# Kernel optimization log

Measured on AMD Instinct MI355X. Metric: run time of the kernel, lower is better.

The kernel has to match this reference:

```python
import jax, jax.numpy as jnp
import numpy as np

N, E = 50000, 800000
DIN, DH, DOUT, HEADS = 128, 128, 128, 4
NEG_SLOPE = 0.2
LN_EPS = 1e-5


def setup_inputs() -> dict:
    key = jax.random.key(0)
    ks = jax.random.split(key, 20)
    s = 0.05
    inp = {
        "x": jax.random.normal(ks[0], (N, DIN), jnp.float32),
        "edge_index": jax.random.randint(ks[1], (2, E), 0, N, jnp.int32),
        "W_in": jax.random.normal(ks[2], (DIN, DH), jnp.float32) * s,
        "b_in": jnp.zeros((DH,), jnp.float32),
        # GAT layer 0 (heads=4, concat)
        "W0": jax.random.normal(ks[3], (DH, DH), jnp.float32) * s,
        "as0": jax.random.normal(ks[4], (HEADS, DH // HEADS), jnp.float32) * s,
        "ad0": jax.random.normal(ks[5], (HEADS, DH // HEADS), jnp.float32) * s,
        "b0": jnp.zeros((DH,), jnp.float32),
        # GAT layer 1 (heads=4, concat)
        "W1": jax.random.normal(ks[6], (DH, DH), jnp.float32) * s,
        "as1": jax.random.normal(ks[7], (HEADS, DH // HEADS), jnp.float32) * s,
        "ad1": jax.random.normal(ks[8], (HEADS, DH // HEADS), jnp.float32) * s,
        "b1": jnp.zeros((DH,), jnp.float32),
        # GAT layer 2 (heads=1, no concat)
        "W2": jax.random.normal(ks[9], (DH, DOUT), jnp.float32) * s,
        "as2": jax.random.normal(ks[10], (1, DOUT), jnp.float32) * s,
        "ad2": jax.random.normal(ks[11], (1, DOUT), jnp.float32) * s,
        "b2": jnp.zeros((DOUT,), jnp.float32),
    }
    return inp


def layer_norm(x):
    mu = jnp.mean(x, -1, keepdims=True)
    var = jnp.var(x, -1, keepdims=True)
    return (x - mu) * jax.lax.rsqrt(var + LN_EPS)


def gat_conv(x, src, dst, W, a_src, a_dst, bias, heads, concat):
    # x: [N, D_in]; src/dst include self-loops
    n = x.shape[0]
    c = W.shape[1] // heads
    h = (x @ W).reshape(n, heads, c)                       # [N,H,C]
    al_s = jnp.sum(h * a_src[None], -1)                    # [N,H]
    al_d = jnp.sum(h * a_dst[None], -1)                    # [N,H]
    e = jax.nn.leaky_relu(al_s[src] + al_d[dst], NEG_SLOPE)  # [Etot,H]
    m = jax.ops.segment_max(e, dst, num_segments=n)
    ex = jnp.exp(e - m[dst])
    z = jax.ops.segment_sum(ex, dst, num_segments=n)
    alpha = ex / (z[dst] + 1e-16)                          # [Etot,H]
    out = jax.ops.segment_sum(h[src] * alpha[:, :, None], dst, num_segments=n)  # [N,H,C]
    out = out.reshape(n, heads * c) if concat else jnp.mean(out, 1)
    return out + bias


def reference(x, edge_index, W_in, b_in, W0, as0, ad0, b0,
              W1, as1, ad1, b1, W2, as2, ad2, b2):
    n = x.shape[0]
    loop = jnp.arange(n, dtype=edge_index.dtype)
    src = jnp.concatenate([edge_index[0], loop])  # PyG GATConv adds self-loops
    dst = jnp.concatenate([edge_index[1], loop])

    h = jax.nn.relu(x @ W_in + b_in)  # dropout is identity in eval mode

    res = h
    h = gat_conv(h, src, dst, W0, as0, ad0, b0, HEADS, True)
    h = layer_norm(jax.nn.elu(h) + res)

    res = h
    h = gat_conv(h, src, dst, W1, as1, ad1, b1, HEADS, True)
    h = layer_norm(jax.nn.elu(h) + res)

    h = gat_conv(h, src, dst, W2, as2, ad2, b2, 1, False)
    return layer_norm(h)
```

## Files before the change

### kernel.cpp

```cpp
#include <hip/hip_runtime.h>
#include <hip/hip_bf16.h>

typedef unsigned short ushort_t;
typedef unsigned int uint_t;
typedef __attribute__((ext_vector_type(8))) short short8;
typedef __attribute__((ext_vector_type(4))) float f32x4;
typedef __attribute__((ext_vector_type(2))) float f32x2;

__device__ __forceinline__ ushort_t f2bf(float f) {
    uint_t u = __float_as_uint(f);
    uint_t r = (u + 0x7FFFu + ((u >> 16) & 1u)) >> 16;
    return (ushort_t)r;
}
__device__ __forceinline__ float bf2f_lo(uint_t u) { return __uint_as_float(u << 16); }
__device__ __forceinline__ float bf2f_hi(uint_t u) { return __uint_as_float(u & 0xffff0000u); }
__device__ __forceinline__ f32x2 bf2x2(uint_t u) {
    f32x2 r;
    r.x = __uint_as_float(u << 16);
    r.y = __uint_as_float(u);
    return r;
}
__device__ __forceinline__ f32x2 pk_fma(f32x2 a, f32x2 b, f32x2 c) {
    f32x2 d;
    asm("v_pk_fma_f32 %0, %1, %2, %3" : "=v"(d) : "v"(a), "v"(b), "v"(c));
    return d;
}

#define BSH 8
#define BCK 256
#define CSR_CAP 6144
#define EPB 4096

__global__ void prep_kernel(const float* __restrict__ W_in,
                            const float* __restrict__ W0, const float* __restrict__ as0,
                            const float* __restrict__ ad0,
                            const float* __restrict__ W1, const float* __restrict__ as1,
                            const float* __restrict__ ad1,
                            const float* __restrict__ W2, const float* __restrict__ as2,
                            const float* __restrict__ ad2,
                            ushort_t* __restrict__ BfIn, ushort_t* __restrict__ Bf0,
                            ushort_t* __restrict__ Bf1, ushort_t* __restrict__ Bf2,
                            const int* __restrict__ ei, int* __restrict__ bhist,
                            int E, int N) {
    __shared__ int hist[256];
    int b = blockIdx.x;
    if (b < 35) {
        const float *W, *a_s, *a_d;
        ushort_t* Bf;
        int H, NT, nt;
        if (b < 8)       { W = W_in; a_s = nullptr; a_d = nullptr; Bf = BfIn; H = 0; NT = 8; nt = b; }
        else if (b < 17) { W = W0; a_s = as0; a_d = ad0; Bf = Bf0; H = 4; NT = 9; nt = b - 8; }
        else if (b < 26) { W = W1; a_s = as1; a_d = ad1; Bf = Bf1; H = 4; NT = 9; nt = b - 17; }
        else             { W = W2; a_s = as2; a_d = ad2; Bf = Bf2; H = 1; NT = 9; nt = b - 26; }
        int l = threadIdx.x & 63;
        int ks = threadIdx.x >> 6;
        int kb = ks * 32 + (l >> 4) * 8;
        int col = l & 15;
        ushort_t v[8];
        if (nt < 8) {
#pragma unroll
            for (int j = 0; j < 8; ++j)
                v[j] = f2bf(W[(size_t)(kb + j) * 128 + nt * 16 + col]);
        } else {
#pragma unroll
            for (int j = 0; j < 8; ++j) {
                int k = kb + j;
                float s = 0.f;
                if (H == 4) {
                    if (col < 4) {
                        for (int c = 0; c < 32; ++c)
                            s += W[(size_t)k * 128 + col * 32 + c] * a_s[col * 32 + c];
                    } else if (col < 8) {
                        int h = col - 4;
                        for (int c = 0; c < 32; ++c)
                            s += W[(size_t)k * 128 + h * 32 + c] * a_d[h * 32 + c];
                    }
                } else {
                    if (col == 0) {
                        for (int c = 0; c < 128; ++c) s += W[(size_t)k * 128 + c] * a_s[c];
                    } else if (col == 1) {
                        for (int c = 0; c < 128; ++c) s += W[(size_t)k * 128 + c] * a_d[c];
                    }
                }
                v[j] = f2bf(s);
            }
        }
        uint4 u;
        u.x = (uint_t)v[0] | ((uint_t)v[1] << 16);
        u.y = (uint_t)v[2] | ((uint_t)v[3] << 16);
        u.z = (uint_t)v[4] | ((uint_t)v[5] << 16);
        u.w = (uint_t)v[6] | ((uint_t)v[7] << 16);
        *(uint4*)(Bf + ((size_t)(ks * NT + nt) * 64 + l) * 8) = u;
    } else {
        int tid = threadIdx.x;
        int blk = b - 35;
        hist[tid] = 0;
        __syncthreads();
        int base = blk * EPB;
        int Etot = E + N;
#pragma unroll
        for (int r = 0; r < EPB / 256; ++r) {
            int i = base + r * 256 + tid;
            if (i < Etot) {
                int dst = (i < E) ? ei[E + i] : (i - E);
                atomicAdd(&hist[dst >> BSH], 1);
            }
        }
        __syncthreads();
        bhist[blk * 256 + tid] = hist[tid];
    }
}

__global__ void csr_scan1(const int* __restrict__ bhist, int* __restrict__ obase,
                          int* __restrict__ gtot, int NBLK) {
    __shared__ int ws[4];
    int b = blockIdx.x;
    int t = threadIdx.x;
    int v = (t < NBLK) ? bhist[t * 256 + b] : 0;
    int lane = t & 63, w = t >> 6;
    int x = v;
#pragma unroll
    for (int off = 1; off < 64; off <<= 1) {
        int t2 = __shfl_up(x, off, 64);
        if (lane >= off) x += t2;
    }
    if (lane == 63) ws[w] = x;
    __syncthreads();
    int add = 0;
    for (int j = 0; j < w; ++j) add += ws[j];
    int excl = add + x - v;
    if (t < NBLK) obase[t * 256 + b] = excl;
    if (t == 255) gtot[b] = excl + v;
}

__global__ void csr_scan2(const int* __restrict__ gtot, int* __restrict__ gbase,
                          int* __restrict__ rowp, int N, int Etot) {
    __shared__ int ws[4];
    int t = threadIdx.x;
    int v = gtot[t];
    int lane = t & 63, w = t >> 6;
    int x = v;
#pragma unroll
    for (int off = 1; off < 64; off <<= 1) {
        int t2 = __shfl_up(x, off, 64);
        if (lane >= off) x += t2;
    }
    if (lane == 63) ws[w] = x;
    __syncthreads();
    int add = 0;
    for (int j = 0; j < w; ++j) add += ws[j];
    gbase[t] = add + x - v;
    if (t == 0) {
        gbase[256] = Etot;
        rowp[N] = Etot;
    }
}

__global__ void csr_scatter(const int* __restrict__ ei, const int* __restrict__ gbase,
                            const int* __restrict__ obase, uint2* __restrict__ pairs,
                            int E, int N) {
    __shared__ int cur[256];
    int tid = threadIdx.x;
    int blk = blockIdx.x;
    cur[tid] = gbase[tid] + obase[blk * 256 + tid];
    __syncthreads();
    int base = blk * EPB;
    int Etot = E + N;
#pragma unroll
    for (int r = 0; r < EPB / 256; ++r) {
        int i = base + r * 256 + tid;
        if (i < Etot) {
            int src = (i < E) ? ei[i] : (i - E);
            int dst = (i < E) ? ei[E + i] : (i - E);
            int pos = atomicAdd(&cur[dst >> BSH], 1);
            uint2 p;
            p.x = (uint_t)src;
            p.y = (uint_t)dst;
            pairs[pos] = p;
        }
    }
}

__global__ void bucket_csr(const uint2* __restrict__ pairs, const int* __restrict__ gbase,
                           int* __restrict__ rowp, int* __restrict__ csrc, int N) {
    __shared__ int cnt[256];
    __shared__ int ws[4];
    __shared__ int stage[CSR_CAP];
    int b = blockIdx.x, tid = threadIdx.x;
    int eBeg = gbase[b], eEnd = gbase[b + 1];
    int M = eEnd - eBeg;
    cnt[tid] = 0;
    __syncthreads();
    for (int t = tid; t < M; t += 256) {
        uint2 pr = pairs[eBeg + t];
        atomicAdd(&cnt[pr.y & (BCK - 1)], 1);
    }
    __syncthreads();
    int v = cnt[tid];
    int lane = tid & 63, w = tid >> 6;
    int x = v;
#pragma unroll
    for (int off = 1; off < 64; off <<= 1) {
        int t2 = __shfl_up(x, off, 64);
        if (lane >= off) x += t2;
    }
    if (lane == 63) ws[w] = x;
    __syncthreads();
    int add = 0;
    for (int j = 0; j < w; ++j) add += ws[j];
    int excl = add + x - v;
    int node = (b << BSH) + tid;
    if (node < N) rowp[node] = eBeg + excl;
    __syncthreads();
    cnt[tid] = excl;
    __syncthreads();
    for (int t = tid; t < M; t += 256) {
        uint2 pr = pairs[eBeg + t];
        int pos = atomicAdd(&cnt[pr.y & (BCK - 1)], 1);
        if (pos < CSR_CAP) stage[pos] = (int)pr.x;
        else csrc[eBeg + pos] = (int)pr.x;
    }
    __syncthreads();
    int lim = (M < CSR_CAP) ? M : CSR_CAP;
    for (int t = tid; t < lim; t += 256) csrc[eBeg + t] = stage[t];
}

template <int MODE>
__device__ __forceinline__ void gemm_epilogue(f32x4* acc, int r0, int lg, int lc,
                                              const float* bias, ushort_t* outB,
                                              float* alS, float* alD) {
    if (MODE == 0) {
#pragma unroll
        for (int r = 0; r < 4; ++r) {
            int row = r0 + lg * 4 + r;
            ushort_t* op = outB + (size_t)row * 128 + lc;
#pragma unroll
            for (int nt = 0; nt < 8; ++nt) {
                float v = fmaxf(acc[nt][r] + bias[nt * 16 + lc], 0.f);
                op[nt * 16] = f2bf(v);
            }
        }
    } else {
#pragma unroll
        for (int r = 0; r < 4; ++r) {
            int row = r0 + lg * 4 + r;
            ushort_t* op = outB + (size_t)row * 128 + lc;
#pragma unroll
            for (int nt = 0; nt < 8; ++nt) op[nt * 16] = f2bf(acc[nt][r]);
            float lv = acc[8][r];
            if (MODE == 1) {
                if (lc < 4) alS[(size_t)row * 4 + lc] = lv;
                else if (lc < 8) alD[(size_t)row * 4 + (lc - 4)] = lv;
            } else {
                if (lc == 0) alS[row] = lv;
                else if (lc == 1) alD[row] = lv;
            }
        }
    }
}

template <int MODE>
__launch_bounds__(256)
__global__ void gemm_mfma(const float* __restrict__ Af, const ushort_t* __restrict__ Ab,
                          const ushort_t* __restrict__ Bf, const float* __restrict__ bias,
                          ushort_t* __restrict__ outB, float* __restrict__ alS,
                          float* __restrict__ alD, int M) {
    const int NT = (MODE == 0) ? 8 : 9;
    __shared__ ushort_t Bs[4 * 9 * 64 * 8];
    {
        const int tot = 4 * NT * 64;
        for (int t = threadIdx.x; t < tot; t += 256)
            ((uint4*)Bs)[t] = ((const uint4*)Bf)[t];
    }
    __syncthreads();

    int wid = threadIdx.x >> 6, l = threadIdx.x & 63;
    int lg = l >> 4, lc = l & 15;
    int r0 = (blockIdx.x * 4 + wid) * 32;
    if (r0 >= M) return;
    bool has1 = (r0 + 16) < M;
    int rowA0 = r0 + lc;
    int rowA1 = has1 ? (r0 + 16 + lc) : rowA0;

    f32x4 acc0[9], acc1[9];
#pragma unroll
    for (int nt = 0; nt < NT; ++nt) {
        acc0[nt] = (f32x4){0.f, 0.f, 0.f, 0.f};
        acc1[nt] = (f32x4){0.f, 0.f, 0.f, 0.f};
    }

#pragma unroll
    for (int ks = 0; ks < 4; ++ks) {
        int k0 = ks * 32 + lg * 8;
        short8 af0, af1;
        if (MODE == 0) {
            const float* ap0 = Af + (size_t)rowA0 * 128 + k0;
            const float* ap1 = Af + (size_t)rowA1 * 128 + k0;
            float4 x0 = *(const float4*)ap0;
            float4 x1 = *(const float4*)(ap0 + 4);
            float4 y0 = *(const float4*)ap1;
            float4 y1 = *(const float4*)(ap1 + 4);
            af0[0] = (short)f2bf(x0.x); af0[1] = (short)f2bf(x0.y);
            af0[2] = (short)f2bf(x0.z); af0[3] = (short)f2bf(x0.w);
            af0[4] = (short)f2bf(x1.x); af0[5] = (short)f2bf(x1.y);
            af0[6] = (short)f2bf(x1.z); af0[7] = (short)f2bf(x1.w);
            af1[0] = (short)f2bf(y0.x); af1[1] = (short)f2bf(y0.y);
            af1[2] = (short)f2bf(y0.z); af1[3] = (short)f2bf(y0.w);
            af1[4] = (short)f2bf(y1.x); af1[5] = (short)f2bf(y1.y);
            af1[6] = (short)f2bf(y1.z); af1[7] = (short)f2bf(y1.w);
        } else {
            af0 = *(const short8*)(Ab + (size_t)rowA0 * 128 + k0);
            af1 = *(const short8*)(Ab + (size_t)rowA1 * 128 + k0);
        }
#pragma unroll
        for (int nt = 0; nt < NT; ++nt) {
            short8 bfr = *(const short8*)(Bs + ((size_t)(ks * NT + nt) * 64 + l) * 8);
            acc0[nt] = __builtin_amdgcn_mfma_f32_16x16x32_bf16(af0, bfr, acc0[nt], 0, 0, 0);
            acc1[nt] = __builtin_amdgcn_mfma_f32_16x16x32_bf16(af1, bfr, acc1[nt], 0, 0, 0);
        }
    }

    gemm_epilogue<MODE>(acc0, r0, lg, lc, bias, outB, alS, alD);
    if (has1) gemm_epilogue<MODE>(acc1, r0 + 16, lg, lc, bias, outB, alS, alD);
}

template <int H, int FINAL>
__launch_bounds__(256)
__global__ void gat_aggregate(const ushort_t* __restrict__ hWb,
                              const float* __restrict__ alS,
                              const float* __restrict__ alD,
                              const int* __restrict__ rowp,
                              const int* __restrict__ csrc,
                              const float* __restrict__ bias,
                              const ushort_t* __restrict__ resb,
                              ushort_t* __restrict__ outb,
                              float* __restrict__ outf, int n) {
    __shared__ float pbuf[4][64][4];
    __shared__ int obuf[4][64];
    int wid = threadIdx.x >> 6;
    int lane = threadIdx.x & 63;
    int node = blockIdx.x * 4 + wid;
    if (node >= n) return;
    int g = lane >> 4;
    int j = lane & 15;
    int hsel = (H == 4) ? (j >> 2) : 0;
    float ald[4];
    if (H == 4) {
        float4 t = *(const float4*)(alD + (size_t)node * 4);
        ald[0] = t.x; ald[1] = t.y; ald[2] = t.z; ald[3] = t.w;
    } else {
        ald[0] = alD[node];
    }
    int beg = rowp[node], end = rowp[node + 1];
    f32x2 acc2[4];
#pragma unroll
    for (int c = 0; c < 4; ++c) acc2[c] = (f32x2){0.f, 0.f};
    float pz = 0.f;
    const char* hbase = (const char*)hWb;
    int jo = j << 4;

    for (int base = beg; base < end; base += 64) {
        int nc = min(64, end - base);
        if (lane < nc) {
            int s = csrc[base + lane];
            obuf[wid][lane] = s << 8;
            if (H == 4) {
                float4 t = *(const float4*)(alS + (size_t)s * 4);
                float x0 = t.x + ald[0], x1 = t.y + ald[1];
                float x2 = t.z + ald[2], x3 = t.w + ald[3];
                x0 = (x0 > 0.f) ? x0 : 0.2f * x0;
                x1 = (x1 > 0.f) ? x1 : 0.2f * x1;
                x2 = (x2 > 0.f) ? x2 : 0.2f * x2;
                x3 = (x3 > 0.f) ? x3 : 0.2f * x3;
                float4 t4;
                t4.x = __expf(x0); t4.y = __expf(x1);
                t4.z = __expf(x2); t4.w = __expf(x3);
                *(float4*)&pbuf[wid][lane][0] = t4;
            } else {
                float x = alS[s] + ald[0];
                x = (x > 0.f) ? x : 0.2f * x;
                pbuf[wid][lane][0] = __expf(x);
            }
        } else {
            obuf[wid][lane] = node << 8;
            if (H == 4) {
                float4 t4; t4.x = 0.f; t4.y = 0.f; t4.z = 0.f; t4.w = 0.f;
                *(float4*)&pbuf[wid][lane][0] = t4;
            } else {
                pbuf[wid][lane][0] = 0.f;
            }
        }
        int padded = (nc + 7) & ~7;
        for (int i = 0; i < padded; i += 8) {
            int i0 = i + g, i1 = i + 4 + g;
            int o0 = obuf[wid][i0];
            int o1 = obuf[wid][i1];
            float p0 = pbuf[wid][i0][hsel];
            float p1 = pbuf[wid][i1][hsel];
            uint4 h0 = *(const uint4*)(hbase + o0 + jo);
            uint4 h1 = *(const uint4*)(hbase + o1 + jo);
            f32x2 pv0; pv0.x = p0; pv0.y = p0;
            f32x2 pv1; pv1.x = p1; pv1.y = p1;
            acc2[0] = pk_fma(bf2x2(h0.x), pv0, acc2[0]);
            acc2[1] = pk_fma(bf2x2(h0.y), pv0, acc2[1]);
            acc2[2] = pk_fma(bf2x2(h0.z), pv0, acc2[2]);
            acc2[3] = pk_fma(bf2x2(h0.w), pv0, acc2[3]);
            acc2[0] = pk_fma(bf2x2(h1.x), pv1, acc2[0]);
            acc2[1] = pk_fma(bf2x2(h1.y), pv1, acc2[1]);
            acc2[2] = pk_fma(bf2x2(h1.z), pv1, acc2[2]);
            acc2[3] = pk_fma(bf2x2(h1.w), pv1, acc2[3]);
            pz += p0 + p1;
        }
    }

    float acc[8] = {acc2[0].x, acc2[0].y, acc2[1].x, acc2[1].y,
                    acc2[2].x, acc2[2].y, acc2[3].x, acc2[3].y};
#pragma unroll
    for (int c = 0; c < 8; ++c) {
        acc[c] += __shfl_xor(acc[c], 16, 64);
        acc[c] += __shfl_xor(acc[c], 32, 64);
    }
    pz += __shfl_xor(pz, 16, 64);
    pz += __shfl_xor(pz, 32, 64);
    float inv = 1.f / (pz + 1e-16f);

    int c0 = j * 8;
    const float4* bp = (const float4*)(bias + c0);
    float4 bv0 = bp[0], bv1 = bp[1];
    float val[8];
    val[0] = acc[0] * inv + bv0.x; val[1] = acc[1] * inv + bv0.y;
    val[2] = acc[2] * inv + bv0.z; val[3] = acc[3] * inv + bv0.w;
    val[4] = acc[4] * inv + bv1.x; val[5] = acc[5] * inv + bv1.y;
    val[6] = acc[6] * inv + bv1.z; val[7] = acc[7] * inv + bv1.w;
    if (!FINAL) {
        uint4 rv = *((const uint4*)(resb + ((size_t)node << 7)) + j);
        float rr[8] = {bf2f_lo(rv.x), bf2f_hi(rv.x), bf2f_lo(rv.y), bf2f_hi(rv.y),
                       bf2f_lo(rv.z), bf2f_hi(rv.z), bf2f_lo(rv.w), bf2f_hi(rv.w)};
#pragma unroll
        for (int c = 0; c < 8; ++c) {
            float vv = val[c];
            float ev = __expf(vv) - 1.f;
            val[c] = ((vv > 0.f) ? vv : ev) + rr[c];
        }
    }
    float s2 = 0.f;
#pragma unroll
    for (int c = 0; c < 8; ++c) s2 += val[c];
#pragma unroll
    for (int off = 1; off < 16; off <<= 1) s2 += __shfl_xor(s2, off, 64);
    float mean = s2 * (1.f / 128.f);
    float q = 0.f;
    float dd[8];
#pragma unroll
    for (int c = 0; c < 8; ++c) {
        dd[c] = val[c] - mean;
        q += dd[c] * dd[c];
    }
#pragma unroll
    for (int off = 1; off < 16; off <<= 1) q += __shfl_xor(q, off, 64);
    float r = rsqrtf(q * (1.f / 128.f) + 1e-5f);
    if (g == 0) {
        if (FINAL) {
            float* op = outf + ((size_t)node << 7) + c0;
            *(float4*)op = make_float4(dd[0] * r, dd[1] * r, dd[2] * r, dd[3] * r);
            *(float4*)(op + 4) = make_float4(dd[4] * r, dd[5] * r, dd[6] * r, dd[7] * r);
        } else {
            uint4 u;
            u.x = (uint_t)f2bf(dd[0] * r) | ((uint_t)f2bf(dd[1] * r) << 16);
            u.y = (uint_t)f2bf(dd[2] * r) | ((uint_t)f2bf(dd[3] * r) << 16);
            u.z = (uint_t)f2bf(dd[4] * r) | ((uint_t)f2bf(dd[5] * r) << 16);
            u.w = (uint_t)f2bf(dd[6] * r) | ((uint_t)f2bf(dd[7] * r) << 16);
            *((uint4*)(outb + ((size_t)node << 7)) + j) = u;
        }
    }
}

extern "C" void kernel_launch(void* const* d_in, const int* in_sizes, int n_in,
                              void* d_out, int out_size, void* d_ws, size_t ws_size,
                              hipStream_t stream) {
    const int N = in_sizes[0] / 128;
    const int E = in_sizes[1] / 2;
    const int Etot = E + N;
    const int NB = (N + BCK - 1) / BCK;
    const int NBLK = (Etot + EPB - 1) / EPB;

    const float* x    = (const float*)d_in[0];
    const int*   ei   = (const int*)d_in[1];
    const float* W_in = (const float*)d_in[2];
    const float* b_in = (const float*)d_in[3];
    const float* W0   = (const float*)d_in[4];
    const float* as0  = (const float*)d_in[5];
    const float* ad0  = (const float*)d_in[6];
    const float* b0   = (const float*)d_in[7];
    const float* W1   = (const float*)d_in[8];
    const float* as1  = (const float*)d_in[9];
    const float* ad1  = (const float*)d_in[10];
    const float* b1   = (const float*)d_in[11];
    const float* W2   = (const float*)d_in[12];
    const float* as2  = (const float*)d_in[13];
    const float* ad2  = (const float*)d_in[14];
    const float* b2   = (const float*)d_in[15];

    char* wsp = (char*)d_ws;
    size_t off = 0;
    auto carve = [&](size_t bytes) -> void* {
        void* p = wsp + off;
        off += (bytes + 255) & ~(size_t)255;
        return p;
    };
    ushort_t* hAb  = (ushort_t*)carve((size_t)N * 128 * 2);
    ushort_t* hBb  = (ushort_t*)carve((size_t)N * 128 * 2);
    ushort_t* hWb  = (ushort_t*)carve((size_t)N * 128 * 2);
    float*    alS  = (float*)carve((size_t)N * 4 * 4);
    float*    alD  = (float*)carve((size_t)N * 4 * 4);
    int*      rowp = (int*)carve((size_t)(N + 1) * 4);
    int*      csrc = (int*)carve((size_t)Etot * 4);
    int*      bhist= (int*)carve((size_t)NBLK * 256 * 4);
    int*      obase= (int*)carve((size_t)NBLK * 256 * 4);
    int*      gbase= (int*)carve((size_t)257 * 4);
    int*      gtot = (int*)carve((size_t)256 * 4);
    ushort_t* BfIn = (ushort_t*)carve((size_t)4 * 8 * 64 * 8 * 2);
    ushort_t* Bf0  = (ushort_t*)carve((size_t)4 * 9 * 64 * 8 * 2);
    ushort_t* Bf1  = (ushort_t*)carve((size_t)4 * 9 * 64 * 8 * 2);
    ushort_t* Bf2  = (ushort_t*)carve((size_t)4 * 9 * 64 * 8 * 2);
    uint2*    pairs = (uint2*)hWb;
    (void)ws_size; (void)n_in; (void)out_size;

    prep_kernel<<<35 + NBLK, 256, 0, stream>>>(W_in, W0, as0, ad0, W1, as1, ad1,
                                               W2, as2, ad2, BfIn, Bf0, Bf1, Bf2,
                                               ei, bhist, E, N);
    csr_scan1<<<256, 256, 0, stream>>>(bhist, obase, gtot, NBLK);
    csr_scan2<<<1, 256, 0, stream>>>(gtot, gbase, rowp, N, Etot);
    csr_scatter<<<NBLK, 256, 0, stream>>>(ei, gbase, obase, pairs, E, N);
    bucket_csr<<<NB, 256, 0, stream>>>(pairs, gbase, rowp, csrc, N);

    int gg = (N + 127) / 128;
    int ga = (N + 3) / 4;

    gemm_mfma<0><<<gg, 256, 0, stream>>>(x, nullptr, BfIn, b_in, hAb,
                                         nullptr, nullptr, N);
    gemm_mfma<1><<<gg, 256, 0, stream>>>(nullptr, hAb, Bf0, nullptr, hWb, alS, alD, N);
    gat_aggregate<4, 0><<<ga, 256, 0, stream>>>(hWb, alS, alD, rowp, csrc, b0,
                                                hAb, hBb, nullptr, N);
    gemm_mfma<1><<<gg, 256, 0, stream>>>(nullptr, hBb, Bf1, nullptr, hWb, alS, alD, N);
    gat_aggregate<4, 0><<<ga, 256, 0, stream>>>(hWb, alS, alD, rowp, csrc, b1,
                                                hBb, hAb, nullptr, N);
    gemm_mfma<2><<<gg, 256, 0, stream>>>(nullptr, hAb, Bf2, nullptr, hWb, alS, alD, N);
    gat_aggregate<1, 1><<<ga, 256, 0, stream>>>(hWb, alS, alD, rowp, csrc, b2,
                                                nullptr, nullptr, (float*)d_out, N);
}
```

Before: 225.1 us.

## Fuse weight prep into GEMMs and software-pipeline aggregate gathers

Removes the separate prep kernel. Each GEMM block now converts the fp32 weights to bf16 MFMA layout directly in shared memory, and the input GEMM is merged with the edge histogram pass into one launch. This saves a kernel launch and the global round trip for the prepared weights. In exchange, every GEMM block redoes the conversion, including the attention-vector dot products. The aggregate loop also prefetches the next pair of neighbour rows, using padded LDS slots that are zero-filled, so gather latency overlaps the FMAs.

```diff
diff --git a/kernel.cpp b/kernel.cpp
--- a/kernel.cpp
+++ b/kernel.cpp
@@ -31,31 +31,17 @@
 #define CSR_CAP 6144
 #define EPB 4096
 
-__global__ void prep_kernel(const float* __restrict__ W_in,
-                            const float* __restrict__ W0, const float* __restrict__ as0,
-                            const float* __restrict__ ad0,
-                            const float* __restrict__ W1, const float* __restrict__ as1,
-                            const float* __restrict__ ad1,
-                            const float* __restrict__ W2, const float* __restrict__ as2,
-                            const float* __restrict__ ad2,
-                            ushort_t* __restrict__ BfIn, ushort_t* __restrict__ Bf0,
-                            ushort_t* __restrict__ Bf1, ushort_t* __restrict__ Bf2,
-                            const int* __restrict__ ei, int* __restrict__ bhist,
-                            int E, int N) {
-    __shared__ int hist[256];
-    int b = blockIdx.x;
-    if (b < 35) {
-        const float *W, *a_s, *a_d;
-        ushort_t* Bf;
-        int H, NT, nt;
-        if (b < 8)       { W = W_in; a_s = nullptr; a_d = nullptr; Bf = BfIn; H = 0; NT = 8; nt = b; }
-        else if (b < 17) { W = W0; a_s = as0; a_d = ad0; Bf = Bf0; H = 4; NT = 9; nt = b - 8; }
-        else if (b < 26) { W = W1; a_s = as1; a_d = ad1; Bf = Bf1; H = 4; NT = 9; nt = b - 17; }
-        else             { W = W2; a_s = as2; a_d = ad2; Bf = Bf2; H = 1; NT = 9; nt = b - 26; }
-        int l = threadIdx.x & 63;
-        int ks = threadIdx.x >> 6;
-        int kb = ks * 32 + (l >> 4) * 8;
-        int col = l & 15;
+template <int MODE>
+__device__ __forceinline__ void stage_B(ushort_t* Bs, const float* __restrict__ W,
+                                        const float* __restrict__ a_s,
+                                        const float* __restrict__ a_d, int tid) {
+    const int NT = (MODE == 0) ? 8 : 9;
+    int l = tid & 63;
+    int ks = tid >> 6;
+    int kb = ks * 32 + ((l >> 4) * 8);
+    int col = l & 15;
+#pragma unroll
+    for (int nt = 0; nt < NT; ++nt) {
         ushort_t v[8];
         if (nt < 8) {
 #pragma unroll
@@ -66,7 +52,7 @@
             for (int j = 0; j < 8; ++j) {
                 int k = kb + j;
                 float s = 0.f;
-                if (H == 4) {
+                if (MODE == 1) {
                     if (col < 4) {
                         for (int c = 0; c < 32; ++c)
                             s += W[(size_t)k * 128 + col * 32 + c] * a_s[col * 32 + c];
@@ -90,139 +76,8 @@
         u.y = (uint_t)v[2] | ((uint_t)v[3] << 16);
         u.z = (uint_t)v[4] | ((uint_t)v[5] << 16);
         u.w = (uint_t)v[6] | ((uint_t)v[7] << 16);
-        *(uint4*)(Bf + ((size_t)(ks * NT + nt) * 64 + l) * 8) = u;
-    } else {
-        int tid = threadIdx.x;
-        int blk = b - 35;
-        hist[tid] = 0;
-        __syncthreads();
-        int base = blk * EPB;
-        int Etot = E + N;
-#pragma unroll
-        for (int r = 0; r < EPB / 256; ++r) {
-            int i = base + r * 256 + tid;
-            if (i < Etot) {
-                int dst = (i < E) ? ei[E + i] : (i - E);
-                atomicAdd(&hist[dst >> BSH], 1);
-            }
-        }
-        __syncthreads();
-        bhist[blk * 256 + tid] = hist[tid];
-    }
-}
-
-__global__ void csr_scan1(const int* __restrict__ bhist, int* __restrict__ obase,
-                          int* __restrict__ gtot, int NBLK) {
-    __shared__ int ws[4];
-    int b = blockIdx.x;
-    int t = threadIdx.x;
-    int v = (t < NBLK) ? bhist[t * 256 + b] : 0;
-    int lane = t & 63, w = t >> 6;
-    int x = v;
-#pragma unroll
-    for (int off = 1; off < 64; off <<= 1) {
-        int t2 = __shfl_up(x, off, 64);
-        if (lane >= off) x += t2;
-    }
-    if (lane == 63) ws[w] = x;
-    __syncthreads();
-    int add = 0;
-    for (int j = 0; j < w; ++j) add += ws[j];
-    int excl = add + x - v;
-    if (t < NBLK) obase[t * 256 + b] = excl;
-    if (t == 255) gtot[b] = excl + v;
-}
-
-__global__ void csr_scan2(const int* __restrict__ gtot, int* __restrict__ gbase,
-                          int* __restrict__ rowp, int N, int Etot) {
-    __shared__ int ws[4];
-    int t = threadIdx.x;
-    int v = gtot[t];
-    int lane = t & 63, w = t >> 6;
-    int x = v;
-#pragma unroll
-    for (int off = 1; off < 64; off <<= 1) {
-        int t2 = __shfl_up(x, off, 64);
-        if (lane >= off) x += t2;
-    }
-    if (lane == 63) ws[w] = x;
-    __syncthreads();
-    int add = 0;
-    for (int j = 0; j < w; ++j) add += ws[j];
-    gbase[t] = add + x - v;
-    if (t == 0) {
-        gbase[256] = Etot;
-        rowp[N] = Etot;
-    }
-}
-
-__global__ void csr_scatter(const int* __restrict__ ei, const int* __restrict__ gbase,
-                            const int* __restrict__ obase, uint2* __restrict__ pairs,
-                            int E, int N) {
-    __shared__ int cur[256];
-    int tid = threadIdx.x;
-    int blk = blockIdx.x;
-    cur[tid] = gbase[tid] + obase[blk * 256 + tid];
-    __syncthreads();
-    int base = blk * EPB;
-    int Etot = E + N;
-#pragma unroll
-    for (int r = 0; r < EPB / 256; ++r) {
-        int i = base + r * 256 + tid;
-        if (i < Etot) {
-            int src = (i < E) ? ei[i] : (i - E);
-            int dst = (i < E) ? ei[E + i] : (i - E);
-            int pos = atomicAdd(&cur[dst >> BSH], 1);
-            uint2 p;
-            p.x = (uint_t)src;
-            p.y = (uint_t)dst;
-            pairs[pos] = p;
-        }
-    }
-}
-
-__global__ void bucket_csr(const uint2* __restrict__ pairs, const int* __restrict__ gbase,
-                           int* __restrict__ rowp, int* __restrict__ csrc, int N) {
-    __shared__ int cnt[256];
-    __shared__ int ws[4];
-    __shared__ int stage[CSR_CAP];
-    int b = blockIdx.x, tid = threadIdx.x;
-    int eBeg = gbase[b], eEnd = gbase[b + 1];
-    int M = eEnd - eBeg;
-    cnt[tid] = 0;
-    __syncthreads();
-    for (int t = tid; t < M; t += 256) {
-        uint2 pr = pairs[eBeg + t];
-        atomicAdd(&cnt[pr.y & (BCK - 1)], 1);
-    }
-    __syncthreads();
-    int v = cnt[tid];
-    int lane = tid & 63, w = tid >> 6;
-    int x = v;
-#pragma unroll
-    for (int off = 1; off < 64; off <<= 1) {
-        int t2 = __shfl_up(x, off, 64);
-        if (lane >= off) x += t2;
-    }
-    if (lane == 63) ws[w] = x;
-    __syncthreads();
-    int add = 0;
-    for (int j = 0; j < w; ++j) add += ws[j];
-    int excl = add + x - v;
-    int node = (b << BSH) + tid;
-    if (node < N) rowp[node] = eBeg + excl;
-    __syncthreads();
-    cnt[tid] = excl;
-    __syncthreads();
-    for (int t = tid; t < M; t += 256) {
-        uint2 pr = pairs[eBeg + t];
-        int pos = atomicAdd(&cnt[pr.y & (BCK - 1)], 1);
-        if (pos < CSR_CAP) stage[pos] = (int)pr.x;
-        else csrc[eBeg + pos] = (int)pr.x;
-    }
-    __syncthreads();
-    int lim = (M < CSR_CAP) ? M : CSR_CAP;
-    for (int t = tid; t < lim; t += 256) csrc[eBeg + t] = stage[t];
+        *(uint4*)(Bs + ((size_t)(ks * NT + nt) * 64 + l) * 8) = u;
+    }
 }
 
 template <int MODE>
@@ -260,23 +115,16 @@
 }
 
 template <int MODE>
-__launch_bounds__(256)
-__global__ void gemm_mfma(const float* __restrict__ Af, const ushort_t* __restrict__ Ab,
-                          const ushort_t* __restrict__ Bf, const float* __restrict__ bias,
-                          ushort_t* __restrict__ outB, float* __restrict__ alS,
-                          float* __restrict__ alD, int M) {
+__device__ __forceinline__ void gemm_body(ushort_t* Bs, const float* __restrict__ Af,
+                                          const ushort_t* __restrict__ Ab,
+                                          const float* __restrict__ bias,
+                                          ushort_t* __restrict__ outB,
+                                          float* __restrict__ alS, float* __restrict__ alD,
+                                          int gblk, int tid, int M) {
     const int NT = (MODE == 0) ? 8 : 9;
-    __shared__ ushort_t Bs[4 * 9 * 64 * 8];
-    {
-        const int tot = 4 * NT * 64;
-        for (int t = threadIdx.x; t < tot; t += 256)
-            ((uint4*)Bs)[t] = ((const uint4*)Bf)[t];
-    }
-    __syncthreads();
-
-    int wid = threadIdx.x >> 6, l = threadIdx.x & 63;
+    int wid = tid >> 6, l = tid & 63;
     int lg = l >> 4, lc = l & 15;
-    int r0 = (blockIdx.x * 4 + wid) * 32;
+    int r0 = (gblk * 4 + wid) * 32;
     if (r0 >= M) return;
     bool has1 = (r0 + 16) < M;
     int rowA0 = r0 + lc;
@@ -288,7 +136,6 @@
         acc0[nt] = (f32x4){0.f, 0.f, 0.f, 0.f};
         acc1[nt] = (f32x4){0.f, 0.f, 0.f, 0.f};
     }
-
 #pragma unroll
     for (int ks = 0; ks < 4; ++ks) {
         int k0 = ks * 32 + lg * 8;
@@ -319,9 +166,166 @@
             acc1[nt] = __builtin_amdgcn_mfma_f32_16x16x32_bf16(af1, bfr, acc1[nt], 0, 0, 0);
         }
     }
-
     gemm_epilogue<MODE>(acc0, r0, lg, lc, bias, outB, alS, alD);
     if (has1) gemm_epilogue<MODE>(acc1, r0 + 16, lg, lc, bias, outB, alS, alD);
+}
+
+__launch_bounds__(256)
+__global__ void fused0(const float* __restrict__ x, const float* __restrict__ W_in,
+                       const float* __restrict__ b_in, ushort_t* __restrict__ hAb,
+                       const int* __restrict__ ei, int* __restrict__ bhist,
+                       int E, int N, int NBLK, int M) {
+    __shared__ ushort_t shm[4 * 9 * 64 * 8];
+    int b = blockIdx.x;
+    int tid = threadIdx.x;
+    if (b < NBLK) {
+        int* hist = (int*)shm;
+        hist[tid] = 0;
+        __syncthreads();
+        int base = b * EPB;
+        int Etot = E + N;
+#pragma unroll
+        for (int r = 0; r < EPB / 256; ++r) {
+            int i = base + r * 256 + tid;
+            if (i < Etot) {
+                int dst = (i < E) ? ei[E + i] : (i - E);
+                atomicAdd(&hist[dst >> BSH], 1);
+            }
+        }
+        __syncthreads();
+        bhist[b * 256 + tid] = hist[tid];
+    } else {
+        stage_B<0>(shm, W_in, nullptr, nullptr, tid);
+        __syncthreads();
+        gemm_body<0>(shm, x, nullptr, b_in, hAb, nullptr, nullptr, b - NBLK, tid, M);
+    }
+}
+
+template <int MODE>
+__launch_bounds__(256)
+__global__ void gemm_mfma(const ushort_t* __restrict__ Ab, const float* __restrict__ W,
+                          const float* __restrict__ a_s, const float* __restrict__ a_d,
+                          ushort_t* __restrict__ outB, float* __restrict__ alS,
+                          float* __restrict__ alD, int M) {
+    __shared__ ushort_t Bs[4 * 9 * 64 * 8];
+    stage_B<MODE>(Bs, W, a_s, a_d, threadIdx.x);
+    __syncthreads();
+    gemm_body<MODE>(Bs, nullptr, Ab, nullptr, outB, alS, alD,
+                    blockIdx.x, threadIdx.x, M);
+}
+
+__global__ void csr_scan1(const int* __restrict__ bhist, int* __restrict__ obase,
+                          int* __restrict__ gtot, int NBLK) {
+    __shared__ int ws[4];
+    int b = blockIdx.x;
+    int t = threadIdx.x;
+    int v = (t < NBLK) ? bhist[t * 256 + b] : 0;
+    int lane = t & 63, w = t >> 6;
+    int x = v;
+#pragma unroll
+    for (int off = 1; off < 64; off <<= 1) {
+        int t2 = __shfl_up(x, off, 64);
+        if (lane >= off) x += t2;
+    }
+    if (lane == 63) ws[w] = x;
+    __syncthreads();
+    int add = 0;
+    for (int j = 0; j < w; ++j) add += ws[j];
+    int excl = add + x - v;
+    if (t < NBLK) obase[t * 256 + b] = excl;
+    if (t == 255) gtot[b] = excl + v;
+}
+
+__global__ void csr_scan2(const int* __restrict__ gtot, int* __restrict__ gbase,
+                          int* __restrict__ rowp, int N, int Etot) {
+    __shared__ int ws[4];
+    int t = threadIdx.x;
+    int v = gtot[t];
+    int lane = t & 63, w = t >> 6;
+    int x = v;
+#pragma unroll
+    for (int off = 1; off < 64; off <<= 1) {
+        int t2 = __shfl_up(x, off, 64);
+        if (lane >= off) x += t2;
+    }
+    if (lane == 63) ws[w] = x;
+    __syncthreads();
+    int add = 0;
+    for (int j = 0; j < w; ++j) add += ws[j];
+    gbase[t] = add + x - v;
+    if (t == 0) {
+        gbase[256] = Etot;
+        rowp[N] = Etot;
+    }
+}
+
+__global__ void csr_scatter(const int* __restrict__ ei, const int* __restrict__ gbase,
+                            const int* __restrict__ obase, uint2* __restrict__ pairs,
+                            int E, int N) {
+    __shared__ int cur[256];
+    int tid = threadIdx.x;
+    int blk = blockIdx.x;
+    cur[tid] = gbase[tid] + obase[blk * 256 + tid];
+    __syncthreads();
+    int base = blk * EPB;
+    int Etot = E + N;
+#pragma unroll
+    for (int r = 0; r < EPB / 256; ++r) {
+        int i = base + r * 256 + tid;
+        if (i < Etot) {
+            int src = (i < E) ? ei[i] : (i - E);
+            int dst = (i < E) ? ei[E + i] : (i - E);
+            int pos = atomicAdd(&cur[dst >> BSH], 1);
+            uint2 p;
+            p.x = (uint_t)src;
+            p.y = (uint_t)dst;
+            pairs[pos] = p;
+        }
+    }
+}
+
+__global__ void bucket_csr(const uint2* __restrict__ pairs, const int* __restrict__ gbase,
+                           int* __restrict__ rowp, int* __restrict__ csrc, int N) {
+    __shared__ int cnt[256];
+    __shared__ int ws[4];
+    __shared__ int stage[CSR_CAP];
+    int b = blockIdx.x, tid = threadIdx.x;
+    int eBeg = gbase[b], eEnd = gbase[b + 1];
+    int M = eEnd - eBeg;
+    cnt[tid] = 0;
+    __syncthreads();
+    for (int t = tid; t < M; t += 256) {
+        uint2 pr = pairs[eBeg + t];
+        atomicAdd(&cnt[pr.y & (BCK - 1)], 1);
+    }
+    __syncthreads();
+    int v = cnt[tid];
+    int lane = tid & 63, w = tid >> 6;
+    int x = v;
+#pragma unroll
+    for (int off = 1; off < 64; off <<= 1) {
+        int t2 = __shfl_up(x, off, 64);
+        if (lane >= off) x += t2;
+    }
+    if (lane == 63) ws[w] = x;
+    __syncthreads();
+    int add = 0;
+    for (int j = 0; j < w; ++j) add += ws[j];
+    int excl = add + x - v;
+    int node = (b << BSH) + tid;
+    if (node < N) rowp[node] = eBeg + excl;
+    __syncthreads();
+    cnt[tid] = excl;
+    __syncthreads();
+    for (int t = tid; t < M; t += 256) {
+        uint2 pr = pairs[eBeg + t];
+        int pos = atomicAdd(&cnt[pr.y & (BCK - 1)], 1);
+        if (pos < CSR_CAP) stage[pos] = (int)pr.x;
+        else csrc[eBeg + pos] = (int)pr.x;
+    }
+    __syncthreads();
+    int lim = (M < CSR_CAP) ? M : CSR_CAP;
+    for (int t = tid; t < lim; t += 256) csrc[eBeg + t] = stage[t];
 }
 
 template <int H, int FINAL>
@@ -335,8 +339,8 @@
                               const ushort_t* __restrict__ resb,
                               ushort_t* __restrict__ outb,
                               float* __restrict__ outf, int n) {
-    __shared__ float pbuf[4][64][4];
-    __shared__ int obuf[4][64];
+    __shared__ float pbuf[4][72][4];
+    __shared__ int obuf[4][72];
     int wid = threadIdx.x >> 6;
     int lane = threadIdx.x & 63;
     int node = blockIdx.x * 4 + wid;
@@ -350,6 +354,11 @@
         ald[0] = t.x; ald[1] = t.y; ald[2] = t.z; ald[3] = t.w;
     } else {
         ald[0] = alD[node];
+    }
+    if (lane < 8) {
+        obuf[wid][64 + lane] = node << 8;
+        float4 z4; z4.x = 0.f; z4.y = 0.f; z4.z = 0.f; z4.w = 0.f;
+        *(float4*)&pbuf[wid][64 + lane][0] = z4;
     }
     int beg = rowp[node], end = rowp[node + 1];
     f32x2 acc2[4];
@@ -391,14 +400,17 @@
             }
         }
         int padded = (nc + 7) & ~7;
+        int s0 = g, s1 = 4 + g;
+        uint4 h0 = *(const uint4*)(hbase + obuf[wid][s0] + jo);
+        uint4 h1 = *(const uint4*)(hbase + obuf[wid][s1] + jo);
+        float p0 = pbuf[wid][s0][hsel];
+        float p1 = pbuf[wid][s1][hsel];
         for (int i = 0; i < padded; i += 8) {
-            int i0 = i + g, i1 = i + 4 + g;
-            int o0 = obuf[wid][i0];
-            int o1 = obuf[wid][i1];
-            float p0 = pbuf[wid][i0][hsel];
-            float p1 = pbuf[wid][i1][hsel];
-            uint4 h0 = *(const uint4*)(hbase + o0 + jo);
-            uint4 h1 = *(const uint4*)(hbase + o1 + jo);
+            int n0 = i + 8 + g, n1 = i + 12 + g;
+            uint4 g0v = *(const uint4*)(hbase + obuf[wid][n0] + jo);
+            uint4 g1v = *(const uint4*)(hbase + obuf[wid][n1] + jo);
+            float q0 = pbuf[wid][n0][hsel];
+            float q1 = pbuf[wid][n1][hsel];
             f32x2 pv0; pv0.x = p0; pv0.y = p0;
             f32x2 pv1; pv1.x = p1; pv1.y = p1;
             acc2[0] = pk_fma(bf2x2(h0.x), pv0, acc2[0]);
@@ -410,6 +422,7 @@
             acc2[2] = pk_fma(bf2x2(h1.z), pv1, acc2[2]);
             acc2[3] = pk_fma(bf2x2(h1.w), pv1, acc2[3]);
             pz += p0 + p1;
+            h0 = g0v; h1 = g1v; p0 = q0; p1 = q1;
         }
     }
 
@@ -519,33 +532,26 @@
     int*      obase= (int*)carve((size_t)NBLK * 256 * 4);
     int*      gbase= (int*)carve((size_t)257 * 4);
     int*      gtot = (int*)carve((size_t)256 * 4);
-    ushort_t* BfIn = (ushort_t*)carve((size_t)4 * 8 * 64 * 8 * 2);
-    ushort_t* Bf0  = (ushort_t*)carve((size_t)4 * 9 * 64 * 8 * 2);
-    ushort_t* Bf1  = (ushort_t*)carve((size_t)4 * 9 * 64 * 8 * 2);
-    ushort_t* Bf2  = (ushort_t*)carve((size_t)4 * 9 * 64 * 8 * 2);
     uint2*    pairs = (uint2*)hWb;
     (void)ws_size; (void)n_in; (void)out_size;
 
-    prep_kernel<<<35 + NBLK, 256, 0, stream>>>(W_in, W0, as0, ad0, W1, as1, ad1,
-                                               W2, as2, ad2, BfIn, Bf0, Bf1, Bf2,
-                                               ei, bhist, E, N);
+    int gg = (N + 127) / 128;
+    int ga = (N + 3) / 4;
+
+    fused0<<<NBLK + gg, 256, 0, stream>>>(x, W_in, b_in, hAb, ei, bhist,
+                                          E, N, NBLK, N);
     csr_scan1<<<256, 256, 0, stream>>>(bhist, obase, gtot, NBLK);
     csr_scan2<<<1, 256, 0, stream>>>(gtot, gbase, rowp, N, Etot);
     csr_scatter<<<NBLK, 256, 0, stream>>>(ei, gbase, obase, pairs, E, N);
     bucket_csr<<<NB, 256, 0, stream>>>(pairs, gbase, rowp, csrc, N);
 
-    int gg = (N + 127) / 128;
-    int ga = (N + 3) / 4;
-
-    gemm_mfma<0><<<gg, 256, 0, stream>>>(x, nullptr, BfIn, b_in, hAb,
-                                         nullptr, nullptr, N);
-    gemm_mfma<1><<<gg, 256, 0, stream>>>(nullptr, hAb, Bf0, nullptr, hWb, alS, alD, N);
+    gemm_mfma<1><<<gg, 256, 0, stream>>>(hAb, W0, as0, ad0, hWb, alS, alD, N);
     gat_aggregate<4, 0><<<ga, 256, 0, stream>>>(hWb, alS, alD, rowp, csrc, b0,
                                                 hAb, hBb, nullptr, N);
-    gemm_mfma<1><<<gg, 256, 0, stream>>>(nullptr, hBb, Bf1, nullptr, hWb, alS, alD, N);
+    gemm_mfma<1><<<gg, 256, 0, stream>>>(hBb, W1, as1, ad1, hWb, alS, alD, N);
     gat_aggregate<4, 0><<<ga, 256, 0, stream>>>(hWb, alS, alD, rowp, csrc, b1,
                                                 hBb, hAb, nullptr, N);
-    gemm_mfma<2><<<gg, 256, 0, stream>>>(nullptr, hAb, Bf2, nullptr, hWb, alS, alD, N);
+    gemm_mfma<2><<<gg, 256, 0, stream>>>(hAb, W2, as2, ad2, hWb, alS, alD, N);
     gat_aggregate<1, 1><<<ga, 256, 0, stream>>>(hWb, alS, alD, rowp, csrc, b2,
                                                 nullptr, nullptr, (float*)d_out, N);
 }
```

Result: slower. 264.7 us (+17.6%).
